# Performance work log

Measured on AMD Instinct MI355X. Metric: run time of the kernel, lower is better.

## Reference

```python
import jax, jax.numpy as jnp
import numpy as np

ALPHA_U = 1.0 / 10.0   # dt/tauu
ALPHA_V = 1.0 / 150.0  # dt/tauv
M = 10.0

def setup_inputs() -> dict:
    key = jax.random.key(0)
    ks = jax.random.split(key, 6)
    B, D_in, H = 8192, 1024, 2048
    stdv = 1.0 / np.sqrt(H)
    return {
        "x": jax.random.normal(ks[0], (B, D_in), dtype=jnp.float32),
        "u": jax.random.normal(ks[1], (B, H), dtype=jnp.float32),
        "v": jax.random.normal(ks[2], (B, H), dtype=jnp.float32),
        "win": jax.random.uniform(ks[3], (H, D_in), dtype=jnp.float32, minval=-stdv, maxval=stdv),
        "wr": jax.random.uniform(ks[4], (H, H), dtype=jnp.float32, minval=-stdv, maxval=stdv),
        "bias": jax.random.uniform(ks[5], (H,), dtype=jnp.float32, minval=-stdv, maxval=stdv),
    }

def reference(x, u, v, win, wr, bias):
    # v update: leaky blend toward m*u, then relu
    v_new = jax.nn.relu((1.0 - ALPHA_V) * v + (ALPHA_V * M) * u)
    # u update: leaky blend with input + recurrent drive minus adapted v
    drive = jnp.einsum('bi,hi->bh', x, win) + jnp.einsum('bk,hk->bh', u, wr) + bias - v_new
    u_new = jax.nn.relu((1.0 - ALPHA_U) * u + ALPHA_U * drive)
    return (u_new, v_new)
```

## Files before the change

kernel.cpp:

```cpp
#include <hip/hip_runtime.h>
#include <hip/hip_bf16.h>
#include <stdint.h>

#define B_DIM 8192
#define D_IN  1024
#define H_DIM 2048
#define K_DIM (D_IN + H_DIM)

#define CV_CONST  (1.0f - 1.0f/150.0f)
#define CUV_CONST (10.0f/150.0f)
#define CU_CONST  0.9f
#define AU_CONST  0.1f

typedef __attribute__((ext_vector_type(8))) short short8;
typedef __attribute__((ext_vector_type(4))) float floatx4;

__device__ __forceinline__ unsigned short f2bf(float f) {
    union { float f; unsigned u; } x; x.f = f;
    unsigned r = x.u + 0x7fffu + ((x.u >> 16) & 1u);
    return (unsigned short)(r >> 16);
}

#define N4_X   ((B_DIM * D_IN)  / 4)
#define N4_U   ((B_DIM * H_DIM) / 4)
#define N4_WIN ((H_DIM * D_IN)  / 4)
#define N4_WR  ((H_DIM * H_DIM) / 4)
#define N4_TOT (N4_X + N4_U + N4_WIN + N4_WR)

__global__ __launch_bounds__(256)
void pack_all(const float4* __restrict__ x, const float4* __restrict__ u,
              const float4* __restrict__ win, const float4* __restrict__ wr,
              unsigned short* __restrict__ Abf, unsigned short* __restrict__ Wbf) {
    int i = blockIdx.x * 256 + threadIdx.x;
    const float4* src; unsigned short* dst; int shift, mask, coloff;
    if (i < N4_X)                    { src = x;   dst = Abf; shift = 10; mask = 1023; coloff = 0;    }
    else if (i < N4_X + N4_U)        { i -= N4_X; src = u;   dst = Abf; shift = 11; mask = 2047; coloff = D_IN; }
    else if (i < N4_X + N4_U + N4_WIN){ i -= N4_X + N4_U; src = win; dst = Wbf; shift = 10; mask = 1023; coloff = 0; }
    else                             { i -= N4_X + N4_U + N4_WIN; src = wr; dst = Wbf; shift = 11; mask = 2047; coloff = D_IN; }
    int idx = i << 2;
    int r = idx >> shift;
    int c = idx & mask;
    float4 f = src[i];
    ushort4 o;
    o.x = f2bf(f.x); o.y = f2bf(f.y); o.z = f2bf(f.z); o.w = f2bf(f.w);
    *(ushort4*)(dst + (size_t)r * K_DIM + coloff + c) = o;
}

#define GLOAD_LDS16(gp, lp)                                                          \
    __builtin_amdgcn_global_load_lds(                                                \
        (const __attribute__((address_space(1))) unsigned int*)(gp),                 \
        (__attribute__((address_space(3))) unsigned int*)(lp), 16, 0, 0)

#define ES_STRIDE 68
#define ES_REGION (16 * ES_STRIDE)
#define SMEM_BYTES (8 * ES_REGION * 4)

__global__ __launch_bounds__(256, 4)
void gemm_fused(const unsigned short* __restrict__ A,
                const unsigned short* __restrict__ Wc,
                const float* __restrict__ u_in,
                const float* __restrict__ v_in,
                const float* __restrict__ bias,
                float* __restrict__ out)
{
    __shared__ __align__(16) unsigned char smem_raw[SMEM_BYTES];
    unsigned short* As = (unsigned short*)smem_raw;
    unsigned short* Bs = As + 128 * 32;
    float* Esf = (float*)smem_raw;

    const int tid  = threadIdx.x;
    const int wave = tid >> 6;
    const int lane = tid & 63;

    const int bid = blockIdx.x;
    const int wid = ((bid & 7) << 7) | (bid >> 3);
    const int bm = wid >> 4;
    const int bn = wid & 15;

    const int srow = lane >> 2;
    const int gcar = ((lane & 3) - ((lane >> 3) & 3)) & 3;
    const int scol = gcar * 8;
    const unsigned short* Ag = A  + (size_t)(bm * 128 + wave * 32 + srow) * K_DIM + scol;
    const unsigned short* Bg = Wc + (size_t)(bn * 128 + wave * 32 + srow) * K_DIM + scol;
    unsigned short* AsW = As + wave * 1024;
    unsigned short* BsW = Bs + wave * 1024;

    const int wm = (wave >> 1) * 64;
    const int wn = (wave & 1) * 64;
    const int frow = lane & 15;
    const int g    = lane >> 4;
    const int swz  = ((g + (frow >> 1)) & 3) * 8;

    floatx4 acc[4][4] = {};

    for (int k0 = 0; k0 < K_DIM; k0 += 32) {
        GLOAD_LDS16(Ag + k0,              AsW);
        GLOAD_LDS16(Ag + 16 * K_DIM + k0, AsW + 512);
        GLOAD_LDS16(Bg + k0,              BsW);
        GLOAD_LDS16(Bg + 16 * K_DIM + k0, BsW + 512);
        __syncthreads();

        short8 af[4], bfr[4];
#pragma unroll
        for (int i = 0; i < 4; i++)
            af[i] = *(const short8*)&As[(wm + i * 16 + frow) * 32 + swz];
#pragma unroll
        for (int j = 0; j < 4; j++)
            bfr[j] = *(const short8*)&Bs[(wn + j * 16 + frow) * 32 + swz];

#pragma unroll
        for (int i = 0; i < 4; i++)
#pragma unroll
            for (int j = 0; j < 4; j++)
                acc[i][j] = __builtin_amdgcn_mfma_f32_16x16x32_bf16(
                    af[i], bfr[j], acc[i][j], 0, 0, 0);
        __syncthreads();
    }

    const int q   = lane >> 4;
    const int c16 = lane & 15;
    const int rbase = q * 4;
    const int colg = bn * 128 + wn + c16 * 4;
    const float4 b4 = *(const float4*)&bias[colg];
    const size_t outV = (size_t)B_DIM * H_DIM;

#pragma unroll
    for (int i = 0; i < 4; i++) {
        float* Es = Esf + (wave * 2 + (i & 1)) * ES_REGION;
#pragma unroll
        for (int j = 0; j < 4; j++)
#pragma unroll
            for (int r = 0; r < 4; r++)
                Es[(rbase + r) * ES_STRIDE + j * 16 + c16] = acc[i][j][r];
#pragma unroll
        for (int rg = 0; rg < 4; rg++) {
            const int rloc = rg * 4 + q;
            const float4 a4 = *(const float4*)&Es[rloc * ES_STRIDE + c16 * 4];
            const size_t idx = (size_t)(bm * 128 + wm + i * 16 + rloc) * H_DIM + colg;
            const float4 u4 = *(const float4*)&u_in[idx];
            const float4 v4 = *(const float4*)&v_in[idx];
            float4 vn, un;
            vn.x = fmaxf(CV_CONST * v4.x + CUV_CONST * u4.x, 0.0f);
            vn.y = fmaxf(CV_CONST * v4.y + CUV_CONST * u4.y, 0.0f);
            vn.z = fmaxf(CV_CONST * v4.z + CUV_CONST * u4.z, 0.0f);
            vn.w = fmaxf(CV_CONST * v4.w + CUV_CONST * u4.w, 0.0f);
            un.x = fmaxf(CU_CONST * u4.x + AU_CONST * (a4.x + b4.x - vn.x), 0.0f);
            un.y = fmaxf(CU_CONST * u4.y + AU_CONST * (a4.y + b4.y - vn.y), 0.0f);
            un.z = fmaxf(CU_CONST * u4.z + AU_CONST * (a4.z + b4.z - vn.z), 0.0f);
            un.w = fmaxf(CU_CONST * u4.w + AU_CONST * (a4.w + b4.w - vn.w), 0.0f);
            *(float4*)&out[idx]        = un;
            *(float4*)&out[outV + idx] = vn;
        }
    }
}

extern "C" void kernel_launch(void* const* d_in, const int* in_sizes, int n_in,
                              void* d_out, int out_size, void* d_ws, size_t ws_size,
                              hipStream_t stream) {
    const float* x    = (const float*)d_in[0];
    const float* u    = (const float*)d_in[1];
    const float* v    = (const float*)d_in[2];
    const float* win  = (const float*)d_in[3];
    const float* wr   = (const float*)d_in[4];
    const float* bias = (const float*)d_in[5];
    float* out = (float*)d_out;

    unsigned short* Abf = (unsigned short*)d_ws;
    unsigned short* Wbf = Abf + (size_t)B_DIM * K_DIM;

    pack_all<<<N4_TOT / 256, 256, 0, stream>>>(
        (const float4*)x, (const float4*)u, (const float4*)win, (const float4*)wr,
        Abf, Wbf);

    gemm_fused<<<1024, 256, 0, stream>>>(Abf, Wbf, u, v, bias, out);
}
```

Before: 401.5 us.

## Fuse fp32-to-bf16 conversion into GEMM and drop separate pack kernel

Removes the pack kernel that converted x, u, win and wr to bf16 in workspace. The GEMM now loads fp32 tiles straight from the inputs into registers, converts them with packed bf16 conversion, and writes them to LDS with the existing swizzle. The next tile's global loads are issued before the current MFMAs, giving a register-prefetch pipeline. This saves the extra write and re-read of the bf16 copies but reads twice as many bytes per tile inside the GEMM, adds conversion ALU work and an extra barrier per iteration, and lowers the occupancy hint from 4 to 3.

Result: slower. 622.3 us (+55.0%).

```diff
diff --git a/kernel.cpp b/kernel.cpp
--- a/kernel.cpp
+++ b/kernel.cpp
@@ -15,51 +15,36 @@
 typedef __attribute__((ext_vector_type(8))) short short8;
 typedef __attribute__((ext_vector_type(4))) float floatx4;
 
-__device__ __forceinline__ unsigned short f2bf(float f) {
-    union { float f; unsigned u; } x; x.f = f;
-    unsigned r = x.u + 0x7fffu + ((x.u >> 16) & 1u);
-    return (unsigned short)(r >> 16);
+#if defined(__has_builtin)
+#if __has_builtin(__builtin_amdgcn_cvt_pk_bf16_f32)
+#define HAVE_CVT_PK_BF16 1
+#endif
+#endif
+
+__device__ __forceinline__ unsigned pk2bf(float a, float b) {
+#ifdef HAVE_CVT_PK_BF16
+    typedef __attribute__((ext_vector_type(2))) __bf16 bf16x2;
+    bf16x2 v = __builtin_amdgcn_cvt_pk_bf16_f32(a, b);
+    union { bf16x2 v; unsigned u; } cv; cv.v = v;
+    return cv.u;
+#else
+    union { float f; unsigned u; } ua, ub; ua.f = a; ub.f = b;
+    unsigned ra = ua.u + 0x7fffu + ((ua.u >> 16) & 1u);
+    unsigned rb = ub.u + 0x7fffu + ((ub.u >> 16) & 1u);
+    return (ra >> 16) | (rb & 0xffff0000u);
+#endif
 }
-
-#define N4_X   ((B_DIM * D_IN)  / 4)
-#define N4_U   ((B_DIM * H_DIM) / 4)
-#define N4_WIN ((H_DIM * D_IN)  / 4)
-#define N4_WR  ((H_DIM * H_DIM) / 4)
-#define N4_TOT (N4_X + N4_U + N4_WIN + N4_WR)
-
-__global__ __launch_bounds__(256)
-void pack_all(const float4* __restrict__ x, const float4* __restrict__ u,
-              const float4* __restrict__ win, const float4* __restrict__ wr,
-              unsigned short* __restrict__ Abf, unsigned short* __restrict__ Wbf) {
-    int i = blockIdx.x * 256 + threadIdx.x;
-    const float4* src; unsigned short* dst; int shift, mask, coloff;
-    if (i < N4_X)                    { src = x;   dst = Abf; shift = 10; mask = 1023; coloff = 0;    }
-    else if (i < N4_X + N4_U)        { i -= N4_X; src = u;   dst = Abf; shift = 11; mask = 2047; coloff = D_IN; }
-    else if (i < N4_X + N4_U + N4_WIN){ i -= N4_X + N4_U; src = win; dst = Wbf; shift = 10; mask = 1023; coloff = 0; }
-    else                             { i -= N4_X + N4_U + N4_WIN; src = wr; dst = Wbf; shift = 11; mask = 2047; coloff = D_IN; }
-    int idx = i << 2;
-    int r = idx >> shift;
-    int c = idx & mask;
-    float4 f = src[i];
-    ushort4 o;
-    o.x = f2bf(f.x); o.y = f2bf(f.y); o.z = f2bf(f.z); o.w = f2bf(f.w);
-    *(ushort4*)(dst + (size_t)r * K_DIM + coloff + c) = o;
-}
-
-#define GLOAD_LDS16(gp, lp)                                                          \
-    __builtin_amdgcn_global_load_lds(                                                \
-        (const __attribute__((address_space(1))) unsigned int*)(gp),                 \
-        (__attribute__((address_space(3))) unsigned int*)(lp), 16, 0, 0)
 
 #define ES_STRIDE 68
 #define ES_REGION (16 * ES_STRIDE)
 #define SMEM_BYTES (8 * ES_REGION * 4)
 
-__global__ __launch_bounds__(256, 4)
-void gemm_fused(const unsigned short* __restrict__ A,
-                const unsigned short* __restrict__ Wc,
+__global__ __launch_bounds__(256, 3)
+void gemm_fused(const float* __restrict__ x,
                 const float* __restrict__ u_in,
                 const float* __restrict__ v_in,
+                const float* __restrict__ win,
+                const float* __restrict__ wr,
                 const float* __restrict__ bias,
                 float* __restrict__ out)
 {
@@ -77,13 +62,23 @@
     const int bm = wid >> 4;
     const int bn = wid & 15;
 
-    const int srow = lane >> 2;
-    const int gcar = ((lane & 3) - ((lane >> 3) & 3)) & 3;
-    const int scol = gcar * 8;
-    const unsigned short* Ag = A  + (size_t)(bm * 128 + wave * 32 + srow) * K_DIM + scol;
-    const unsigned short* Bg = Wc + (size_t)(bn * 128 + wave * 32 + srow) * K_DIM + scol;
-    unsigned short* AsW = As + wave * 1024;
-    unsigned short* BsW = Bs + wave * 1024;
+    const int srow = lane >> 1;
+    const int half = lane & 1;
+    const int trow = wave * 32 + srow;
+    const int cb   = half * 16;
+    const int g0   = half * 2;
+    const int rr   = (trow & 15) >> 1;
+    const int s0   = (g0 + rr) & 3;
+    const int s1   = (g0 + 1 + rr) & 3;
+    unsigned short* AsW0 = As + trow * 32 + s0 * 8;
+    unsigned short* AsW1 = As + trow * 32 + s1 * 8;
+    unsigned short* BsW0 = Bs + trow * 32 + s0 * 8;
+    unsigned short* BsW1 = Bs + trow * 32 + s1 * 8;
+
+    const float* aBaseX = x    + (size_t)(bm * 128 + trow) * D_IN  + cb;
+    const float* aBaseU = u_in + (size_t)(bm * 128 + trow) * H_DIM + cb - D_IN;
+    const float* bBaseW = win  + (size_t)(bn * 128 + trow) * D_IN  + cb;
+    const float* bBaseR = wr   + (size_t)(bn * 128 + trow) * H_DIM + cb - D_IN;
 
     const int wm = (wave >> 1) * 64;
     const int wn = (wave & 1) * 64;
@@ -91,14 +86,41 @@
     const int g    = lane >> 4;
     const int swz  = ((g + (frow >> 1)) & 3) * 8;
 
+    float4 pa[4], pb[4];
+
+    auto loadAB = [&](int k0) {
+        const float* ap = (k0 < D_IN) ? (aBaseX + k0) : (aBaseU + k0);
+        const float* bp = (k0 < D_IN) ? (bBaseW + k0) : (bBaseR + k0);
+#pragma unroll
+        for (int t = 0; t < 4; t++) {
+            pa[t] = *(const float4*)(ap + 4 * t);
+            pb[t] = *(const float4*)(bp + 4 * t);
+        }
+    };
+    auto stageAB = [&]() {
+        uint4 wa0 = { pk2bf(pa[0].x, pa[0].y), pk2bf(pa[0].z, pa[0].w),
+                      pk2bf(pa[1].x, pa[1].y), pk2bf(pa[1].z, pa[1].w) };
+        uint4 wa1 = { pk2bf(pa[2].x, pa[2].y), pk2bf(pa[2].z, pa[2].w),
+                      pk2bf(pa[3].x, pa[3].y), pk2bf(pa[3].z, pa[3].w) };
+        uint4 wb0 = { pk2bf(pb[0].x, pb[0].y), pk2bf(pb[0].z, pb[0].w),
+                      pk2bf(pb[1].x, pb[1].y), pk2bf(pb[1].z, pb[1].w) };
+        uint4 wb1 = { pk2bf(pb[2].x, pb[2].y), pk2bf(pb[2].z, pb[2].w),
+                      pk2bf(pb[3].x, pb[3].y), pk2bf(pb[3].z, pb[3].w) };
+        *(uint4*)AsW0 = wa0;
+        *(uint4*)AsW1 = wa1;
+        *(uint4*)BsW0 = wb0;
+        *(uint4*)BsW1 = wb1;
+    };
+
     floatx4 acc[4][4] = {};
 
-    for (int k0 = 0; k0 < K_DIM; k0 += 32) {
-        GLOAD_LDS16(Ag + k0,              AsW);
-        GLOAD_LDS16(Ag + 16 * K_DIM + k0, AsW + 512);
-        GLOAD_LDS16(Bg + k0,              BsW);
-        GLOAD_LDS16(Bg + 16 * K_DIM + k0, BsW + 512);
-        __syncthreads();
+    loadAB(0);
+    stageAB();
+    __syncthreads();
+
+    for (int k0 = 0; k0 < K_DIM; ) {
+        const int kn = k0 + 32;
+        if (kn < K_DIM) loadAB(kn);
 
         short8 af[4], bfr[4];
 #pragma unroll
@@ -114,8 +136,15 @@
             for (int j = 0; j < 4; j++)
                 acc[i][j] = __builtin_amdgcn_mfma_f32_16x16x32_bf16(
                     af[i], bfr[j], acc[i][j], 0, 0, 0);
+
+        k0 = kn;
+        if (k0 >= K_DIM) break;
+        __syncthreads();
+        stageAB();
         __syncthreads();
     }
+
+    __syncthreads();
 
     const int q   = lane >> 4;
     const int c16 = lane & 15;
@@ -165,12 +194,5 @@
     const float* bias = (const float*)d_in[5];
     float* out = (float*)d_out;
 
-    unsigned short* Abf = (unsigned short*)d_ws;
-    unsigned short* Wbf = Abf + (size_t)B_DIM * K_DIM;
-
-    pack_all<<<N4_TOT / 256, 256, 0, stream>>>(
-        (const float4*)x, (const float4*)u, (const float4*)win, (const float4*)wr,
-        Abf, Wbf);
-
-    gemm_fused<<<1024, 256, 0, stream>>>(Abf, Wbf, u, v, bias, out);
+    gemm_fused<<<1024, 256, 0, stream>>>(x, u, v, win, wr, bias, out);
 }
```
